# Kernel optimization log

Hardware: AMD Instinct MI355X
Metric: run time of the kernel (lower is better)

## Reference

```python
import jax, jax.numpy as jnp
import numpy as np
from jax import lax

# Static module config (matches init_kwargs)
KH, KW = 3, 3
SH, SW = 1, 1
PH, PW = 1, 1
DH, DW = 1, 1
DG = 1           # deformable groups
GROUPS = 1


def setup_inputs() -> dict:
    key = jax.random.key(0)
    k1, k2, k3 = jax.random.split(key, 3)
    B, C, H, W = 8, 256, 64, 64
    Co = 256
    K = KH * KW
    x = jax.random.normal(k1, (B, C, H, W), dtype=jnp.float32)
    # offset/mask conv weight: (2+1)*DG*K = 27 output channels; small so offsets are a few pixels
    w_offset = jax.random.normal(k2, (3 * DG * K, C, KH, KW), dtype=jnp.float32) * 0.05
    # main conv weight, uniform(-stdv, stdv) per reset_parameters
    stdv = 1.0 / np.sqrt(C * KH * KW)
    w_conv = jax.random.uniform(k3, (Co, C, KH, KW), dtype=jnp.float32, minval=-stdv, maxval=stdv)
    return {"input_feat": x, "w_offset": w_offset, "w_conv": w_conv}


def _bilinear_gather(x, py, px):
    """x: (B, DG, Cg, H, W); py/px: (B, DG, K, Ho, Wo) float sample coords.
    Returns sampled values (B, DG, Cg, K, Ho, Wo) with zero padding outside."""
    B, dg, Cg, H, W = x.shape
    _, _, K, Ho, Wo = py.shape
    xf = x.reshape(B, dg, Cg, H * W)

    y0 = jnp.floor(py)
    x0 = jnp.floor(px)
    ly = py - y0
    lx = px - x0
    y0i = y0.astype(jnp.int32)
    x0i = x0.astype(jnp.int32)
    y1i = y0i + 1
    x1i = x0i + 1

    def gather(yi, xi):
        valid = (yi >= 0) & (yi < H) & (xi >= 0) & (xi < W)
        idx = jnp.clip(yi, 0, H - 1) * W + jnp.clip(xi, 0, W - 1)  # (B,dg,K,Ho,Wo)
        idx_f = idx.reshape(B, dg, K * Ho * Wo)
        g = jax.vmap(jax.vmap(lambda f, i: jnp.take(f, i, axis=1)))(xf, idx_f)
        return g.reshape(B, dg, Cg, K, Ho, Wo), valid

    g00, v00 = gather(y0i, x0i)
    g01, v01 = gather(y0i, x1i)
    g10, v10 = gather(y1i, x0i)
    g11, v11 = gather(y1i, x1i)

    w00 = ((1 - ly) * (1 - lx) * v00)[:, :, None]
    w01 = ((1 - ly) * lx * v01)[:, :, None]
    w10 = (ly * (1 - lx) * v10)[:, :, None]
    w11 = (ly * lx * v11)[:, :, None]
    return g00 * w00 + g01 * w01 + g10 * w10 + g11 * w11


def _deform_conv(x, w_offset, w_conv):
    B, C, H, W = x.shape
    Co = w_conv.shape[0]
    K = KH * KW
    dn = ("NCHW", "OIHW", "NCHW")

    # offset/mask branch (regular conv)
    om = lax.conv_general_dilated(x, w_offset, (SH, SW), ((PH, PH), (PW, PW)),
                                  rhs_dilation=(DH, DW), dimension_numbers=dn)
    Ho, Wo = om.shape[2], om.shape[3]
    off_y = om[:, : DG * K].reshape(B, DG, K, Ho, Wo)
    off_x = om[:, DG * K: 2 * DG * K].reshape(B, DG, K, Ho, Wo)
    mask = jax.nn.sigmoid(om[:, 2 * DG * K:]).reshape(B, DG, 1, K, Ho, Wo)

    # base sampling grid
    oy = jnp.arange(Ho) * SH - PH                 # (Ho,)
    ox = jnp.arange(Wo) * SW - PW                 # (Wo,)
    ky = (jnp.arange(KH) * DH)[:, None].repeat(KW, 1).reshape(K)  # (K,)
    kx = (jnp.arange(KW) * DW)[None, :].repeat(KH, 0).reshape(K)  # (K,)
    py = ky[None, None, :, None, None] + oy[None, None, None, :, None] + off_y
    px = kx[None, None, :, None, None] + ox[None, None, None, None, :] + off_x

    xg = x.reshape(B, DG, C // DG, H, W)
    sampled = _bilinear_gather(xg, py, px) * mask  # (B,DG,Cg,K,Ho,Wo)

    cols = sampled.reshape(B, C, K, Ho * Wo)
    wk = w_conv.reshape(Co, C, K)
    out = jnp.einsum("bckn,ock->bon", cols, wk)
    return out.reshape(B, Co, Ho, Wo)


def reference(input_feat, w_offset, w_conv):
    return _deform_conv(input_feat, w_offset, w_conv)
```

## Files before the change

### kernel.cpp

```cpp
#include <hip/hip_runtime.h>
#include <hip/hip_bf16.h>

typedef float f32x4 __attribute__((ext_vector_type(4)));
typedef unsigned int u32x4 __attribute__((ext_vector_type(4)));
typedef __bf16 bf16x8 __attribute__((ext_vector_type(8)));

#define NSP 4096
#define KTOT 2304

static __device__ __forceinline__ float bflo(unsigned u) {
  return __builtin_bit_cast(float, u << 16);
}
static __device__ __forceinline__ float bfhi(unsigned u) {
  return __builtin_bit_cast(float, u & 0xffff0000u);
}
static __device__ __forceinline__ unsigned short bfbits(float f) {
  return __builtin_bit_cast(unsigned short, (__bf16)f);
}
static __device__ __forceinline__ unsigned packbf2(float f0, float f1) {
  return (unsigned)bfbits(f0) | ((unsigned)bfbits(f1) << 16);
}
static __device__ __forceinline__ float bf16f(unsigned short h) {
  return __builtin_bit_cast(float, (unsigned)h << 16);
}

__global__ __launch_bounds__(256) void k_nhwc(const float* __restrict__ x,
                                              unsigned short* __restrict__ XH) {
  const int by = blockIdx.x;
  const int t = threadIdx.x;
  const int xw = t & 63;
  const int cq = t >> 6;
  const float* xp = x + (((by >> 6) * 256 * 64 + (by & 63)) * 64 + xw);
  unsigned short* oh = XH + (by * 64 + xw) * 256;
#pragma unroll
  for (int j8 = 0; j8 < 8; ++j8) {
    const int c0 = cq * 64 + j8 * 8;
    u32x4 vh;
#pragma unroll
    for (int d = 0; d < 4; ++d) {
      float f0 = xp[(c0 + 2 * d) * 4096];
      float f1 = xp[(c0 + 2 * d + 1) * 4096];
      vh[d] = packbf2(f0, f1);
    }
    *(u32x4*)(oh + c0) = vh;
  }
}

__global__ void k_wprep_all(const float* __restrict__ wc, const float* __restrict__ wof,
                            unsigned short* __restrict__ AW2,
                            unsigned short* __restrict__ AF) {
  int idx = blockIdx.x * 256 + threadIdx.x;
  if (idx < 589824) {
    int ks = idx / 16384;
    int r = idx - ks * 16384;
    int chunk = r >> 5;
    int e = r & 31;
    int ah = chunk >> 8, am = chunk & 255;
    int col = (ks >> 2) * 256 + (ks & 3) * 64 + ah * 32 + e;
    int c = col & 255, tap = col >> 8;
    AW2[idx] = bfbits(wc[(am * 256 + c) * 9 + tap]);
  } else {
    int j = idx - 589824;
    if (j < 147456) {
      int skc = j >> 11;
      int r = j & 2047;
      int fi = r >> 9;
      int lane = (r >> 3) & 63;
      int e = r & 7;
      int ks = skc >> 1, kc = skc & 1;
      int tap = ks >> 2, q = ks & 3;
      int mr = lane & 15, ko = (lane >> 4) * 8;
      int m = (fi & 1) * 16 + mr;
      int gcol = tap * 256 + q * 64 + ko + kc * 32 + e;
      int c = gcol & 255;
      int t = gcol >> 8;
      float v = (m < 27) ? wof[(m * 256 + c) * 9 + t] : 0.f;
      unsigned short h = bfbits(v);
      AF[j] = (fi >> 1) ? bfbits(v - bf16f(h)) : h;
    }
  }
}

__global__ __launch_bounds__(256) void k_offc2(const unsigned short* __restrict__ AF,
                                               const unsigned short* __restrict__ XH,
                                               f32x4* __restrict__ W4,
                                               unsigned* __restrict__ C4) {
  __shared__ u32x4 ldsq[1024];
  unsigned char* ldsbase = (unsigned char*)ldsq;
  float* lds32 = (float*)ldsq;

  const int tid = threadIdx.x;
  const int bid = blockIdx.x;
  const int b = bid & 7;
  const int y = bid >> 3;
  const int l = tid & 63;
  const int w = tid >> 6;

  const unsigned short* xb = XH + b * (64 * 64 * 256);
  const int sp = tid >> 2;
  const int qtr = tid & 3;
  const unsigned swb = (unsigned)(sp & 7) << 4;
  const int col = w * 16 + (l & 15);
  const unsigned swc = (unsigned)(col & 7) << 4;

  f32x4 acc0 = (f32x4){0.f, 0.f, 0.f, 0.f};
  f32x4 acc1 = (f32x4){0.f, 0.f, 0.f, 0.f};
  u32x4 v0, v1;

  {
    const int yy = y - 1;
    const int xx = sp - 1;
    const bool valid = ((unsigned)yy < 64u) & ((unsigned)xx < 64u);
    const int yyc = min(max(yy, 0), 63), xxc = min(max(xx, 0), 63);
    const unsigned short* src = xb + ((yyc * 64 + xxc) * 256 + qtr * 16);
    u32x4 z = (u32x4){0u, 0u, 0u, 0u};
    v0 = valid ? *(const u32x4*)src : z;
    v1 = valid ? *(const u32x4*)(src + 8) : z;
    *(u32x4*)(ldsbase + (unsigned)sp * 128u + (((unsigned)(qtr * 32)) ^ swb)) = v0;
    *(u32x4*)(ldsbase + (unsigned)sp * 128u + (((unsigned)(qtr * 32 + 16)) ^ swb)) = v1;
  }

  for (int ks = 0; ks < 36; ++ks) {
    unsigned char* ldsB = ldsbase + (ks & 1) * 8192;
    unsigned char* ldsBn = ldsbase + ((ks & 1) ^ 1) * 8192;
    const bool pf = (ks + 1 < 36);

    if (pf) {
      int tap = (ks + 1) >> 2, q = (ks + 1) & 3;
      int yy = y + tap / 3 - 1, xx = sp + tap % 3 - 1;
      bool valid = ((unsigned)yy < 64u) & ((unsigned)xx < 64u);
      int yyc = min(max(yy, 0), 63), xxc = min(max(xx, 0), 63);
      const unsigned short* src = xb + ((yyc * 64 + xxc) * 256 + q * 64 + qtr * 16);
      u32x4 z = (u32x4){0u, 0u, 0u, 0u};
      v0 = valid ? *(const u32x4*)src : z;
      v1 = valid ? *(const u32x4*)(src + 8) : z;
    }

    asm volatile("s_waitcnt lgkmcnt(0)" ::: "memory");
    __builtin_amdgcn_s_barrier();

    const unsigned short* af = AF + ks * 4096;
#pragma unroll
    for (int kc = 0; kc < 2; ++kc) {
      bf16x8 ah0 = *(const bf16x8*)(af + kc * 2048 + l * 8);
      bf16x8 ah1 = *(const bf16x8*)(af + kc * 2048 + 512 + l * 8);
      bf16x8 al0 = *(const bf16x8*)(af + kc * 2048 + 1024 + l * 8);
      bf16x8 al1 = *(const bf16x8*)(af + kc * 2048 + 1536 + l * 8);
      bf16x8 bh = *(const bf16x8*)(ldsB + (unsigned)col * 128u +
                                   (((unsigned)(kc * 64 + (l >> 4) * 16)) ^ swc));
      acc0 = __builtin_amdgcn_mfma_f32_16x16x32_bf16(ah0, bh, acc0, 0, 0, 0);
      acc1 = __builtin_amdgcn_mfma_f32_16x16x32_bf16(ah1, bh, acc1, 0, 0, 0);
      acc0 = __builtin_amdgcn_mfma_f32_16x16x32_bf16(al0, bh, acc0, 0, 0, 0);
      acc1 = __builtin_amdgcn_mfma_f32_16x16x32_bf16(al1, bh, acc1, 0, 0, 0);
    }

    if (pf) {
      *(u32x4*)(ldsBn + (unsigned)sp * 128u + (((unsigned)(qtr * 32)) ^ swb)) = v0;
      *(u32x4*)(ldsBn + (unsigned)sp * 128u + (((unsigned)(qtr * 32 + 16)) ^ swb)) = v1;
    }
  }

  __syncthreads();
#pragma unroll
  for (int mf = 0; mf < 2; ++mf) {
    f32x4 a = mf ? acc1 : acc0;
#pragma unroll
    for (int r = 0; r < 4; ++r) {
      int m = mf * 16 + (l >> 4) * 4 + r;
      int px = w * 16 + (l & 15);
      lds32[m * 64 + px] = a[r];
    }
  }
  __syncthreads();

#pragma unroll
  for (int it = 0; it < 3; ++it) {
    int idx = tid + it * 256;
    if (idx < 9 * 64) {
      int k = idx >> 6, px = idx & 63;
      float oy = lds32[k * 64 + px];
      float ox = lds32[(9 + k) * 64 + px];
      float lg = lds32[(18 + k) * 64 + px];
      int s = y * 64 + px;
      float py = oy + (float)y - 1.f + (float)(k / 3);
      float pxf = ox + (float)px - 1.f + (float)(k % 3);
      float mk = 1.f / (1.f + __expf(-lg));

      float y0f = floorf(py), x0f = floorf(pxf);
      float ly = py - y0f, lx = pxf - x0f;
      int y0 = (int)y0f, x0 = (int)x0f;
      int y1 = y0 + 1, x1 = x0 + 1;
      float omy = 1.f - ly, omx = 1.f - lx;
      bool y0v = (unsigned)y0 < 64u, y1v = (unsigned)y1 < 64u;
      bool x0v = (unsigned)x0 < 64u, x1v = (unsigned)x1 < 64u;
      f32x4 wv;
      wv[0] = (y0v && x0v) ? omy * omx * mk : 0.f;
      wv[1] = (y0v && x1v) ? omy * lx * mk : 0.f;
      wv[2] = (y1v && x0v) ? ly * omx * mk : 0.f;
      wv[3] = (y1v && x1v) ? ly * lx * mk : 0.f;
      int y0c = min(max(y0, 0), 63), y1c = min(max(y1, 0), 63);
      int x0c = min(max(x0, 0), 63), x1c = min(max(x1, 0), 63);
      unsigned p00 = (unsigned)(y0c * 64 + x0c);
      unsigned p11 = (unsigned)(y1c * 64 + x1c);
      int ci = (b * 9 + k) * NSP + s;
      W4[ci] = wv;
      C4[ci] = p00 | (p11 << 16);
    }
  }
}

struct Bld16 {
  u32x4 g00a, g00b, g01a, g01b, g10a, g10b, g11a, g11b;
  f32x4 wv;
};

static __device__ __forceinline__ void loadMeta(const f32x4* __restrict__ W4,
                                                const unsigned* __restrict__ C4,
                                                int b, int k, int s,
                                                f32x4& wv, unsigned& c4) {
  int ci = (b * 9 + k) * NSP + s;
  wv = W4[ci];
  c4 = C4[ci];
}

static __device__ __forceinline__ void loadCorners(const unsigned short* __restrict__ xb,
                                                   f32x4 wv, unsigned c4, int c0, int bc,
                                                   Bld16& r) {
  r.wv = wv;
  unsigned p00 = c4 & 0xffffu, p11 = c4 >> 16;
  unsigned p01 = (p00 & ~63u) | (p11 & 63u);
  unsigned p10 = (p11 & ~63u) | (p00 & 63u);
  const unsigned short* base = xb + (c0 + bc);
  const unsigned short* q00 = base + (p00 << 8);
  const unsigned short* q01 = base + (p01 << 8);
  const unsigned short* q10 = base + (p10 << 8);
  const unsigned short* q11 = base + (p11 << 8);
  r.g00a = *(const u32x4*)q00;
  r.g00b = *(const u32x4*)(q00 + 8);
  r.g01a = *(const u32x4*)q01;
  r.g01b = *(const u32x4*)(q01 + 8);
  r.g10a = *(const u32x4*)q10;
  r.g10b = *(const u32x4*)(q10 + 8);
  r.g11a = *(const u32x4*)q11;
  r.g11b = *(const u32x4*)(q11 + 8);
}

static __device__ __forceinline__ void blendB16(const Bld16& r, u32x4& o0, u32x4& o1) {
#pragma unroll
  for (int d = 0; d < 4; ++d) {
    float a0 = r.wv[0] * bflo(r.g00a[d]) + r.wv[1] * bflo(r.g01a[d]) +
               r.wv[2] * bflo(r.g10a[d]) + r.wv[3] * bflo(r.g11a[d]);
    float a1 = r.wv[0] * bfhi(r.g00a[d]) + r.wv[1] * bfhi(r.g01a[d]) +
               r.wv[2] * bfhi(r.g10a[d]) + r.wv[3] * bfhi(r.g11a[d]);
    o0[d] = packbf2(a0, a1);
    float b0 = r.wv[0] * bflo(r.g00b[d]) + r.wv[1] * bflo(r.g01b[d]) +
               r.wv[2] * bflo(r.g10b[d]) + r.wv[3] * bflo(r.g11b[d]);
    float b1 = r.wv[0] * bfhi(r.g00b[d]) + r.wv[1] * bfhi(r.g01b[d]) +
               r.wv[2] * bfhi(r.g10b[d]) + r.wv[3] * bfhi(r.g11b[d]);
    o1[d] = packbf2(b0, b1);
  }
}

__global__ __launch_bounds__(512) void k_gemm(const unsigned short* __restrict__ AW2,
                                              const unsigned short* __restrict__ XH,
                                              const f32x4* __restrict__ W4,
                                              const unsigned* __restrict__ C4v,
                                              float* __restrict__ out) {
  __shared__ u32x4 lds2[2][3072];
  unsigned char* ldsbase = (unsigned char*)lds2;

  const int tid = threadIdx.x;
  const int bid = blockIdx.x;
  const int b = bid & 7;
  const int s0 = (bid >> 3) * 128;

  const int l = tid & 63;
  const int w = tid >> 6;
  const int wm = (w >> 1) * 64;
  const int wn = (w & 1) * 64;

  const int am = tid & 255;
  const int ah = tid >> 8;
  const unsigned swa = (unsigned)(am & 7) << 4;

  const int bn = tid >> 2;
  const int bc = (tid & 3) * 16;
  const int s = s0 + bn;
  const unsigned swb = (unsigned)(bn & 7) << 4;
  const unsigned short* xb = XH + b * (64 * 64 * 256);

  f32x4 acc[4][4];
#pragma unroll
  for (int i = 0; i < 4; ++i)
#pragma unroll
    for (int j = 0; j < 4; ++j) acc[i][j] = (f32x4){0.f, 0.f, 0.f, 0.f};

  f32x4 mwvA, mwvB;
  unsigned mc4A, mc4B;
  Bld16 bldA, bldB;
  u32x4 arA[4], arB[4];

  loadMeta(W4, C4v, b, 0, s, mwvA, mc4A);
  loadMeta(W4, C4v, b, 0, s, mwvB, mc4B);
#pragma unroll
  for (int j = 0; j < 4; ++j) arA[j] = *(const u32x4*)(AW2 + tid * 32 + j * 8);
  loadCorners(xb, mwvA, mc4A, 0, bc, bldA);
  loadMeta(W4, C4v, b, 0, s, mwvA, mc4A);
  {
    u32x4 o0, o1;
    blendB16(bldA, o0, o1);
    unsigned char* ldsA = ldsbase;
    unsigned char* ldsB = ldsbase + 32768;
    const unsigned abase = (unsigned)am * 128u;
#pragma unroll
    for (int j = 0; j < 4; ++j)
      *(u32x4*)(ldsA + abase + (((unsigned)(ah * 64 + j * 16)) ^ swa)) = arA[j];
    const unsigned bbase = (unsigned)bn * 128u;
    *(u32x4*)(ldsB + bbase + (((unsigned)(bc * 2)) ^ swb)) = o0;
    *(u32x4*)(ldsB + bbase + (((unsigned)(bc * 2 + 16)) ^ swb)) = o1;
  }
#pragma unroll
  for (int j = 0; j < 4; ++j)
    arB[j] = *(const u32x4*)(AW2 + 16384 + tid * 32 + j * 8);
  loadCorners(xb, mwvB, mc4B, 64, bc, bldB);

  auto mfma_half = [&](unsigned char* ldsA, unsigned char* ldsB, int H) {
    bf16x8 af[4], bfr[4];
    const unsigned co = (unsigned)(H * 64 + ((l >> 4) * 16));
#pragma unroll
    for (int i = 0; i < 4; ++i) {
      int row = wm + i * 16 + (l & 15);
      af[i] = *(const bf16x8*)(ldsA + (unsigned)row * 128u +
                               (co ^ ((unsigned)(row & 7) << 4)));
    }
#pragma unroll
    for (int j = 0; j < 4; ++j) {
      int col = wn + j * 16 + (l & 15);
      bfr[j] = *(const bf16x8*)(ldsB + (unsigned)col * 128u +
                                (co ^ ((unsigned)(col & 7) << 4)));
    }
#pragma unroll
    for (int i = 0; i < 4; ++i)
#pragma unroll
      for (int j = 0; j < 4; ++j)
        acc[i][j] = __builtin_amdgcn_mfma_f32_16x16x32_bf16(af[i], bfr[j],
                                                            acc[i][j], 0, 0, 0);
  };

  auto gstep = [&](int KS, u32x4 (&arI)[4], Bld16& bldI, f32x4& mwvI, unsigned& mc4I,
                   f32x4& mwvO, unsigned& mc4O, u32x4 (&arU)[4], Bld16& bldU) {
    const int cur = KS & 1;
    unsigned char* ldsA = ldsbase + cur * 49152;
    unsigned char* ldsB = ldsA + 32768;
    unsigned char* ldsAn = ldsbase + (cur ^ 1) * 49152;
    unsigned char* ldsBn = ldsAn + 32768;

    if (KS + 2 < 36) {
#pragma unroll
      for (int j = 0; j < 4; ++j)
        arI[j] = *(const u32x4*)(AW2 + (KS + 2) * 16384 + tid * 32 + j * 8);
    }

    asm volatile("s_waitcnt lgkmcnt(0)" ::: "memory");
    __builtin_amdgcn_s_barrier();

    __builtin_amdgcn_s_setprio(1);
    mfma_half(ldsA, ldsB, 0);
    __builtin_amdgcn_s_setprio(0);

    if (KS + 2 < 36)
      loadCorners(xb, mwvI, mc4I, ((KS + 2) & 3) << 6, bc, bldI);
    if (KS + 3 < 36)
      loadMeta(W4, C4v, b, (KS + 3) >> 2, s, mwvO, mc4O);

    __builtin_amdgcn_s_setprio(1);
    mfma_half(ldsA, ldsB, 1);
    __builtin_amdgcn_s_setprio(0);

    if (KS + 1 < 36) {
      u32x4 o0, o1;
      blendB16(bldU, o0, o1);
      const unsigned abase = (unsigned)am * 128u;
#pragma unroll
      for (int j = 0; j < 4; ++j)
        *(u32x4*)(ldsAn + abase + (((unsigned)(ah * 64 + j * 16)) ^ swa)) = arU[j];
      const unsigned bbase = (unsigned)bn * 128u;
      *(u32x4*)(ldsBn + bbase + (((unsigned)(bc * 2)) ^ swb)) = o0;
      *(u32x4*)(ldsBn + bbase + (((unsigned)(bc * 2 + 16)) ^ swb)) = o1;
    }
  };

  for (int ks2 = 0; ks2 < 36; ks2 += 2) {
    gstep(ks2, arA, bldA, mwvA, mc4A, mwvB, mc4B, arB, bldB);
    gstep(ks2 + 1, arB, bldB, mwvB, mc4B, mwvA, mc4A, arA, bldA);
  }

  const int cn2 = l & 15;
  const int r0 = (l >> 4) * 4;
#pragma unroll
  for (int i = 0; i < 4; ++i) {
#pragma unroll
    for (int j = 0; j < 4; ++j) {
      int sc = s0 + wn + j * 16 + cn2;
#pragma unroll
      for (int r = 0; r < 4; ++r) {
        int o = wm + i * 16 + r0 + r;
        out[((b * 256 + o) << 12) + sc] = acc[i][j][r];
      }
    }
  }
}

extern "C" void kernel_launch(void* const* d_in, const int* in_sizes, int n_in,
                              void* d_out, int out_size, void* d_ws, size_t ws_size,
                              hipStream_t stream) {
  const float* x = (const float*)d_in[0];
  const float* wof = (const float*)d_in[1];
  const float* wc = (const float*)d_in[2];
  float* out = (float*)d_out;
  char* ws = (char*)d_ws;

  unsigned short* XH = (unsigned short*)(ws);
  unsigned short* AW2 = (unsigned short*)(ws + 16777216);
  unsigned short* AF = (unsigned short*)(ws + 17956864);
  f32x4* W4 = (f32x4*)(ws + 18251776);
  unsigned* C4 = (unsigned*)(ws + 22970368);

  k_nhwc<<<512, 256, 0, stream>>>(x, XH);
  k_wprep_all<<<2880, 256, 0, stream>>>(wc, wof, AW2, AF);
  k_offc2<<<512, 256, 0, stream>>>(AF, XH, W4, C4);
  k_gemm<<<256, 512, 0, stream>>>(AW2, XH, W4, C4, out);
}
```

Measured before the change: 121.6 us.

## Load weight MFMA fragments directly from global into registers, bypassing LDS

```diff
diff --git a/kernel.cpp b/kernel.cpp
--- a/kernel.cpp
+++ b/kernel.cpp
@@ -47,18 +47,23 @@
 }
 
 __global__ void k_wprep_all(const float* __restrict__ wc, const float* __restrict__ wof,
-                            unsigned short* __restrict__ AW2,
+                            unsigned short* __restrict__ AWF,
                             unsigned short* __restrict__ AF) {
   int idx = blockIdx.x * 256 + threadIdx.x;
   if (idx < 589824) {
     int ks = idx / 16384;
     int r = idx - ks * 16384;
-    int chunk = r >> 5;
-    int e = r & 31;
-    int ah = chunk >> 8, am = chunk & 255;
-    int col = (ks >> 2) * 256 + (ks & 3) * 64 + ah * 32 + e;
+    int mg = r >> 12;
+    int r2 = r & 4095;
+    int kk = r2 >> 11;
+    int r3 = r2 & 2047;
+    int fi = r3 >> 9;
+    int r4 = r3 & 511;
+    int lane = r4 >> 3, e = r4 & 7;
+    int row = mg * 64 + fi * 16 + (lane & 15);
+    int col = ks * 64 + kk * 32 + (lane >> 4) * 8 + e;
     int c = col & 255, tap = col >> 8;
-    AW2[idx] = bfbits(wc[(am * 256 + c) * 9 + tap]);
+    AWF[idx] = bfbits(wc[(row * 256 + c) * 9 + tap]);
   } else {
     int j = idx - 589824;
     if (j < 147456) {
@@ -261,12 +266,12 @@
   }
 }
 
-__global__ __launch_bounds__(512) void k_gemm(const unsigned short* __restrict__ AW2,
+__global__ __launch_bounds__(512) void k_gemm(const unsigned short* __restrict__ AWF,
                                               const unsigned short* __restrict__ XH,
                                               const f32x4* __restrict__ W4,
                                               const unsigned* __restrict__ C4v,
                                               float* __restrict__ out) {
-  __shared__ u32x4 lds2[2][3072];
+  __shared__ u32x4 lds2[2][1024];
   unsigned char* ldsbase = (unsigned char*)lds2;
 
   const int tid = threadIdx.x;
@@ -276,12 +281,9 @@
 
   const int l = tid & 63;
   const int w = tid >> 6;
-  const int wm = (w >> 1) * 64;
+  const int mg = w >> 1;
+  const int wm = mg * 64;
   const int wn = (w & 1) * 64;
-
-  const int am = tid & 255;
-  const int ah = tid >> 8;
-  const unsigned swa = (unsigned)(am & 7) << 4;
 
   const int bn = tid >> 2;
   const int bc = (tid & 3) * 16;
@@ -298,41 +300,29 @@
   f32x4 mwvA, mwvB;
   unsigned mc4A, mc4B;
   Bld16 bldA, bldB;
-  u32x4 arA[4], arB[4];
+  bf16x8 afA[8], afB[8];
 
   loadMeta(W4, C4v, b, 0, s, mwvA, mc4A);
   loadMeta(W4, C4v, b, 0, s, mwvB, mc4B);
-#pragma unroll
-  for (int j = 0; j < 4; ++j) arA[j] = *(const u32x4*)(AW2 + tid * 32 + j * 8);
+  {
+    const unsigned short* ap = AWF + mg * 4096;
+#pragma unroll
+    for (int t = 0; t < 8; ++t) afA[t] = *(const bf16x8*)(ap + t * 512 + l * 8);
+  }
   loadCorners(xb, mwvA, mc4A, 0, bc, bldA);
   loadMeta(W4, C4v, b, 0, s, mwvA, mc4A);
   {
     u32x4 o0, o1;
     blendB16(bldA, o0, o1);
-    unsigned char* ldsA = ldsbase;
-    unsigned char* ldsB = ldsbase + 32768;
-    const unsigned abase = (unsigned)am * 128u;
-#pragma unroll
-    for (int j = 0; j < 4; ++j)
-      *(u32x4*)(ldsA + abase + (((unsigned)(ah * 64 + j * 16)) ^ swa)) = arA[j];
     const unsigned bbase = (unsigned)bn * 128u;
-    *(u32x4*)(ldsB + bbase + (((unsigned)(bc * 2)) ^ swb)) = o0;
-    *(u32x4*)(ldsB + bbase + (((unsigned)(bc * 2 + 16)) ^ swb)) = o1;
-  }
-#pragma unroll
-  for (int j = 0; j < 4; ++j)
-    arB[j] = *(const u32x4*)(AW2 + 16384 + tid * 32 + j * 8);
+    *(u32x4*)(ldsbase + bbase + (((unsigned)(bc * 2)) ^ swb)) = o0;
+    *(u32x4*)(ldsbase + bbase + (((unsigned)(bc * 2 + 16)) ^ swb)) = o1;
+  }
   loadCorners(xb, mwvB, mc4B, 64, bc, bldB);
 
-  auto mfma_half = [&](unsigned char* ldsA, unsigned char* ldsB, int H) {
-    bf16x8 af[4], bfr[4];
+  auto mfma_half = [&](const bf16x8* afU, unsigned char* ldsB, int H) {
+    bf16x8 bfr[4];
     const unsigned co = (unsigned)(H * 64 + ((l >> 4) * 16));
-#pragma unroll
-    for (int i = 0; i < 4; ++i) {
-      int row = wm + i * 16 + (l & 15);
-      af[i] = *(const bf16x8*)(ldsA + (unsigned)row * 128u +
-                               (co ^ ((unsigned)(row & 7) << 4)));
-    }
 #pragma unroll
     for (int j = 0; j < 4; ++j) {
       int col = wn + j * 16 + (l & 15);
@@ -343,29 +333,28 @@
     for (int i = 0; i < 4; ++i)
 #pragma unroll
       for (int j = 0; j < 4; ++j)
-        acc[i][j] = __builtin_amdgcn_mfma_f32_16x16x32_bf16(af[i], bfr[j],
+        acc[i][j] = __builtin_amdgcn_mfma_f32_16x16x32_bf16(afU[H * 4 + i], bfr[j],
                                                             acc[i][j], 0, 0, 0);
   };
 
-  auto gstep = [&](int KS, u32x4 (&arI)[4], Bld16& bldI, f32x4& mwvI, unsigned& mc4I,
-                   f32x4& mwvO, unsigned& mc4O, u32x4 (&arU)[4], Bld16& bldU) {
+  auto gstep = [&](int KS, bf16x8 (&afI)[8], bf16x8 (&afU)[8],
+                   Bld16& bldI, f32x4& mwvI, unsigned& mc4I,
+                   f32x4& mwvO, unsigned& mc4O, Bld16& bldU) {
     const int cur = KS & 1;
-    unsigned char* ldsA = ldsbase + cur * 49152;
-    unsigned char* ldsB = ldsA + 32768;
-    unsigned char* ldsAn = ldsbase + (cur ^ 1) * 49152;
-    unsigned char* ldsBn = ldsAn + 32768;
-
-    if (KS + 2 < 36) {
-#pragma unroll
-      for (int j = 0; j < 4; ++j)
-        arI[j] = *(const u32x4*)(AW2 + (KS + 2) * 16384 + tid * 32 + j * 8);
+    unsigned char* ldsB = ldsbase + cur * 16384;
+    unsigned char* ldsBn = ldsbase + (cur ^ 1) * 16384;
+
+    if (KS + 1 < 36) {
+      const unsigned short* ap = AWF + (KS + 1) * 16384 + mg * 4096;
+#pragma unroll
+      for (int t = 0; t < 8; ++t) afI[t] = *(const bf16x8*)(ap + t * 512 + l * 8);
     }
 
     asm volatile("s_waitcnt lgkmcnt(0)" ::: "memory");
     __builtin_amdgcn_s_barrier();
 
     __builtin_amdgcn_s_setprio(1);
-    mfma_half(ldsA, ldsB, 0);
+    mfma_half(afU, ldsB, 0);
     __builtin_amdgcn_s_setprio(0);
 
     if (KS + 2 < 36)
@@ -374,16 +363,12 @@
       loadMeta(W4, C4v, b, (KS + 3) >> 2, s, mwvO, mc4O);
 
     __builtin_amdgcn_s_setprio(1);
-    mfma_half(ldsA, ldsB, 1);
+    mfma_half(afU, ldsB, 1);
     __builtin_amdgcn_s_setprio(0);
 
     if (KS + 1 < 36) {
       u32x4 o0, o1;
       blendB16(bldU, o0, o1);
-      const unsigned abase = (unsigned)am * 128u;
-#pragma unroll
-      for (int j = 0; j < 4; ++j)
-        *(u32x4*)(ldsAn + abase + (((unsigned)(ah * 64 + j * 16)) ^ swa)) = arU[j];
       const unsigned bbase = (unsigned)bn * 128u;
       *(u32x4*)(ldsBn + bbase + (((unsigned)(bc * 2)) ^ swb)) = o0;
       *(u32x4*)(ldsBn + bbase + (((unsigned)(bc * 2 + 16)) ^ swb)) = o1;
@@ -391,8 +376,8 @@
   };
 
   for (int ks2 = 0; ks2 < 36; ks2 += 2) {
-    gstep(ks2, arA, bldA, mwvA, mc4A, mwvB, mc4B, arB, bldB);
-    gstep(ks2 + 1, arB, bldB, mwvB, mc4B, mwvA, mc4A, arA, bldA);
+    gstep(ks2, afB, afA, bldA, mwvA, mc4A, mwvB, mc4B, bldB);
+    gstep(ks2 + 1, afA, afB, bldB, mwvB, mc4B, mwvA, mc4A, bldA);
   }
 
   const int cn2 = l & 15;
@@ -421,13 +406,13 @@
   char* ws = (char*)d_ws;
 
   unsigned short* XH = (unsigned short*)(ws);
-  unsigned short* AW2 = (unsigned short*)(ws + 16777216);
+  unsigned short* AWF = (unsigned short*)(ws + 16777216);
   unsigned short* AF = (unsigned short*)(ws + 17956864);
   f32x4* W4 = (f32x4*)(ws + 18251776);
   unsigned* C4 = (unsigned*)(ws + 22970368);
 
   k_nhwc<<<512, 256, 0, stream>>>(x, XH);
-  k_wprep_all<<<2880, 256, 0, stream>>>(wc, wof, AW2, AF);
+  k_wprep_all<<<2880, 256, 0, stream>>>(wc, wof, AWF, AF);
   k_offc2<<<512, 256, 0, stream>>>(AF, XH, W4, C4);
-  k_gemm<<<256, 512, 0, stream>>>(AW2, XH, W4, C4, out);
-}
+  k_gemm<<<256, 512, 0, stream>>>(AWF, XH, W4, C4, out);
+}
```

Result: slower. 129.8 us (+6.7%).

## Load GEMM weight tiles directly into LDS with global_load_lds DMA

Applied to the files above, without the earlier changes.

```diff
diff --git a/kernel.cpp b/kernel.cpp
--- a/kernel.cpp
+++ b/kernel.cpp
@@ -22,6 +22,12 @@
 }
 static __device__ __forceinline__ float bf16f(unsigned short h) {
   return __builtin_bit_cast(float, (unsigned)h << 16);
+}
+
+static __device__ __forceinline__ void dma16(const unsigned short* g, unsigned short* l) {
+  __builtin_amdgcn_global_load_lds(
+      (const __attribute__((address_space(1))) unsigned int*)g,
+      (__attribute__((address_space(3))) unsigned int*)l, 16, 0, 0);
 }
 
 __global__ __launch_bounds__(256) void k_nhwc(const float* __restrict__ x,
@@ -47,18 +53,18 @@
 }
 
 __global__ void k_wprep_all(const float* __restrict__ wc, const float* __restrict__ wof,
-                            unsigned short* __restrict__ AW2,
+                            unsigned short* __restrict__ AWL,
                             unsigned short* __restrict__ AF) {
   int idx = blockIdx.x * 256 + threadIdx.x;
   if (idx < 589824) {
     int ks = idx / 16384;
-    int r = idx - ks * 16384;
-    int chunk = r >> 5;
-    int e = r & 31;
-    int ah = chunk >> 8, am = chunk & 255;
-    int col = (ks >> 2) * 256 + (ks & 3) * 64 + ah * 32 + e;
+    int e = idx - ks * 16384;
+    int row = e >> 6;
+    int se = e & 63;
+    int offb = (se * 2) ^ ((row & 7) << 4);
+    int col = ks * 64 + (offb >> 1);
     int c = col & 255, tap = col >> 8;
-    AW2[idx] = bfbits(wc[(am * 256 + c) * 9 + tap]);
+    AWL[idx] = bfbits(wc[(row * 256 + c) * 9 + tap]);
   } else {
     int j = idx - 589824;
     if (j < 147456) {
@@ -261,7 +267,7 @@
   }
 }
 
-__global__ __launch_bounds__(512) void k_gemm(const unsigned short* __restrict__ AW2,
+__global__ __launch_bounds__(512) void k_gemm(const unsigned short* __restrict__ AWL,
                                               const unsigned short* __restrict__ XH,
                                               const f32x4* __restrict__ W4,
                                               const unsigned* __restrict__ C4v,
@@ -279,10 +285,6 @@
   const int wm = (w >> 1) * 64;
   const int wn = (w & 1) * 64;
 
-  const int am = tid & 255;
-  const int ah = tid >> 8;
-  const unsigned swa = (unsigned)(am & 7) << 4;
-
   const int bn = tid >> 2;
   const int bc = (tid & 3) * 16;
   const int s = s0 + bn;
@@ -298,30 +300,25 @@
   f32x4 mwvA, mwvB;
   unsigned mc4A, mc4B;
   Bld16 bldA, bldB;
-  u32x4 arA[4], arB[4];
 
   loadMeta(W4, C4v, b, 0, s, mwvA, mc4A);
   loadMeta(W4, C4v, b, 0, s, mwvB, mc4B);
-#pragma unroll
-  for (int j = 0; j < 4; ++j) arA[j] = *(const u32x4*)(AW2 + tid * 32 + j * 8);
+  {
+    const unsigned short* g0 = AWL + (w * 4) * 512 + l * 8;
+#pragma unroll
+    for (int k = 0; k < 4; ++k)
+      dma16(g0 + k * 512, (unsigned short*)(ldsbase + (unsigned)(w * 4 + k) * 1024u));
+  }
   loadCorners(xb, mwvA, mc4A, 0, bc, bldA);
   loadMeta(W4, C4v, b, 0, s, mwvA, mc4A);
   {
     u32x4 o0, o1;
     blendB16(bldA, o0, o1);
-    unsigned char* ldsA = ldsbase;
     unsigned char* ldsB = ldsbase + 32768;
-    const unsigned abase = (unsigned)am * 128u;
-#pragma unroll
-    for (int j = 0; j < 4; ++j)
-      *(u32x4*)(ldsA + abase + (((unsigned)(ah * 64 + j * 16)) ^ swa)) = arA[j];
     const unsigned bbase = (unsigned)bn * 128u;
     *(u32x4*)(ldsB + bbase + (((unsigned)(bc * 2)) ^ swb)) = o0;
     *(u32x4*)(ldsB + bbase + (((unsigned)(bc * 2 + 16)) ^ swb)) = o1;
   }
-#pragma unroll
-  for (int j = 0; j < 4; ++j)
-    arB[j] = *(const u32x4*)(AW2 + 16384 + tid * 32 + j * 8);
   loadCorners(xb, mwvB, mc4B, 64, bc, bldB);
 
   auto mfma_half = [&](unsigned char* ldsA, unsigned char* ldsB, int H) {
@@ -347,22 +344,22 @@
                                                             acc[i][j], 0, 0, 0);
   };
 
-  auto gstep = [&](int KS, u32x4 (&arI)[4], Bld16& bldI, f32x4& mwvI, unsigned& mc4I,
-                   f32x4& mwvO, unsigned& mc4O, u32x4 (&arU)[4], Bld16& bldU) {
+  auto gstep = [&](int KS, Bld16& bldI, f32x4& mwvI, unsigned& mc4I,
+                   f32x4& mwvO, unsigned& mc4O, Bld16& bldU) {
     const int cur = KS & 1;
     unsigned char* ldsA = ldsbase + cur * 49152;
     unsigned char* ldsB = ldsA + 32768;
     unsigned char* ldsAn = ldsbase + (cur ^ 1) * 49152;
     unsigned char* ldsBn = ldsAn + 32768;
 
-    if (KS + 2 < 36) {
-#pragma unroll
-      for (int j = 0; j < 4; ++j)
-        arI[j] = *(const u32x4*)(AW2 + (KS + 2) * 16384 + tid * 32 + j * 8);
-    }
-
-    asm volatile("s_waitcnt lgkmcnt(0)" ::: "memory");
-    __builtin_amdgcn_s_barrier();
+    __syncthreads();
+
+    if (KS + 1 < 36) {
+      const unsigned short* g0 = AWL + (KS + 1) * 16384 + (w * 4) * 512 + l * 8;
+#pragma unroll
+      for (int k = 0; k < 4; ++k)
+        dma16(g0 + k * 512, (unsigned short*)(ldsAn + (unsigned)(w * 4 + k) * 1024u));
+    }
 
     __builtin_amdgcn_s_setprio(1);
     mfma_half(ldsA, ldsB, 0);
@@ -380,10 +377,6 @@
     if (KS + 1 < 36) {
       u32x4 o0, o1;
       blendB16(bldU, o0, o1);
-      const unsigned abase = (unsigned)am * 128u;
-#pragma unroll
-      for (int j = 0; j < 4; ++j)
-        *(u32x4*)(ldsAn + abase + (((unsigned)(ah * 64 + j * 16)) ^ swa)) = arU[j];
       const unsigned bbase = (unsigned)bn * 128u;
       *(u32x4*)(ldsBn + bbase + (((unsigned)(bc * 2)) ^ swb)) = o0;
       *(u32x4*)(ldsBn + bbase + (((unsigned)(bc * 2 + 16)) ^ swb)) = o1;
@@ -391,8 +384,8 @@
   };
 
   for (int ks2 = 0; ks2 < 36; ks2 += 2) {
-    gstep(ks2, arA, bldA, mwvA, mc4A, mwvB, mc4B, arB, bldB);
-    gstep(ks2 + 1, arB, bldB, mwvB, mc4B, mwvA, mc4A, arA, bldA);
+    gstep(ks2, bldA, mwvA, mc4A, mwvB, mc4B, bldB);
+    gstep(ks2 + 1, bldB, mwvB, mc4B, mwvA, mc4A, bldA);
   }
 
   const int cn2 = l & 15;
@@ -421,13 +414,13 @@
   char* ws = (char*)d_ws;
 
   unsigned short* XH = (unsigned short*)(ws);
-  unsigned short* AW2 = (unsigned short*)(ws + 16777216);
+  unsigned short* AWL = (unsigned short*)(ws + 16777216);
   unsigned short* AF = (unsigned short*)(ws + 17956864);
   f32x4* W4 = (f32x4*)(ws + 18251776);
   unsigned* C4 = (unsigned*)(ws + 22970368);
 
   k_nhwc<<<512, 256, 0, stream>>>(x, XH);
-  k_wprep_all<<<2880, 256, 0, stream>>>(wc, wof, AW2, AF);
+  k_wprep_all<<<2880, 256, 0, stream>>>(wc, wof, AWL, AF);
   k_offc2<<<512, 256, 0, stream>>>(AF, XH, W4, C4);
-  k_gemm<<<256, 512, 0, stream>>>(AW2, XH, W4, C4, out);
-}
+  k_gemm<<<256, 512, 0, stream>>>(AWL, XH, W4, C4, out);
+}
```

Result: faster. 114.6 us (-5.8%).
